# Optimization experiments

Hardware: AMD Instinct MI355X
Metric: run time of the kernel (lower is better)

Reference implementation:

```python
import jax, jax.numpy as jnp
import numpy as np


def _conv1x1(x, w, b):
    # x: [B,C,H,W], w: [O,C], b: [O] -> [B,O,H,W]
    return jnp.einsum('bchw,oc->bohw', x, w) + b[None, :, None, None]


def setup_inputs() -> dict:
    key = jax.random.key(0)
    ks = jax.random.split(key, 11)
    B, C, Ci, H, W = 4, 256, 128, 64, 64
    s_in = 1.0 / np.sqrt(C)
    s_ci = 1.0 / np.sqrt(Ci)
    return {
        'x': jax.random.normal(ks[0], (B, C, H, W), jnp.float32),
        'g_w': jax.random.normal(ks[1], (Ci, C), jnp.float32) * s_in,
        'g_b': jax.random.normal(ks[2], (Ci,), jnp.float32) * 0.01,
        'theta_w': jax.random.normal(ks[3], (Ci, C), jnp.float32) * s_in,
        'theta_b': jax.random.normal(ks[4], (Ci,), jnp.float32) * 0.01,
        'phi_w': jax.random.normal(ks[5], (Ci, C), jnp.float32) * s_in,
        'phi_b': jax.random.normal(ks[6], (Ci,), jnp.float32) * 0.01,
        'wz_w': jax.random.normal(ks[7], (C, Ci), jnp.float32) * s_ci,
        'wz_b': jax.random.normal(ks[8], (C,), jnp.float32) * 0.01,
        'bn_gamma': jax.random.uniform(ks[9], (C,), jnp.float32, 0.5, 1.5),
        'bn_beta': jax.random.normal(ks[10], (C,), jnp.float32) * 0.01,
    }


def reference(x, g_w, g_b, theta_w, theta_b, phi_w, phi_b, wz_w, wz_b, bn_gamma, bn_beta):
    B, C, H, W = x.shape
    Ci = g_w.shape[0]
    N = H * W
    # 1x1 conv projections, flattened over spatial positions
    g_x = _conv1x1(x, g_w, g_b).reshape(B, Ci, N).transpose(0, 2, 1)       # [B,N,Ci]
    theta_x = _conv1x1(x, theta_w, theta_b).reshape(B, Ci, N)              # [B,Ci,N]
    phi_x = _conv1x1(x, phi_w, phi_b).reshape(B, Ci, N)                    # [B,Ci,N]
    # f[b, i, j] = theta_i . phi_j  -> [B,N,N]
    f = jnp.einsum('bci,bcj->bij', theta_x, phi_x)
    # NOTE: softmax over dim=1 (query axis) — faithful to original (non-standard)
    f_div_C = jax.nn.softmax(f, axis=1)
    y = jnp.einsum('bij,bjc->bic', f_div_C, g_x)                           # [B,N,Ci]
    y = y.transpose(0, 2, 1).reshape(B, Ci, H, W)                          # [B,Ci,H,W]
    # W_z: 1x1 conv + BatchNorm2d (training-mode batch statistics)
    w_y = _conv1x1(y, wz_w, wz_b)                                          # [B,C,H,W]
    mean = jnp.mean(w_y, axis=(0, 2, 3), keepdims=True)
    var = jnp.var(w_y, axis=(0, 2, 3), keepdims=True)
    w_y = (w_y - mean) * jax.lax.rsqrt(var + 1e-5)
    w_y = w_y * bn_gamma[None, :, None, None] + bn_beta[None, :, None, None]
    return w_y + x
```

## Files before the change

kernel.cpp:

```cpp
#include <hip/hip_runtime.h>


#define B_  4
#define C_  256
#define CI  128
#define N_  4096
#define NB  (B_*N_)
#define ISPLIT 16
#define MB_ (1u<<20)
#define LOG2E 1.442695041f

typedef _Float16 f16;
typedef f16   f16x8 __attribute__((ext_vector_type(8)));
typedef f16   f16x4 __attribute__((ext_vector_type(4)));
typedef float f32x4 __attribute__((ext_vector_type(4)));
typedef float f32x16 __attribute__((ext_vector_type(16)));
typedef unsigned u32x2 __attribute__((ext_vector_type(2)));
typedef unsigned u32x4v __attribute__((ext_vector_type(4)));

#define MFMA(a,b,c)   __builtin_amdgcn_mfma_f32_16x16x32_f16(a,b,c,0,0,0)
#define MFMA32(a,b,c) __builtin_amdgcn_mfma_f32_32x32x16_f16(a,b,c,0,0,0)

#define GLD16(g, lp) __builtin_amdgcn_global_load_lds( \
    (const __attribute__((address_space(1))) void*)(g), \
    (__attribute__((address_space(3))) void*)(lp), 16, 0, 0)

#define OFF_THETA  0
#define OFF_PHI    (4u*MB_)
#define OFF_G      (8u*MB_)
#define OFF_YP     (12u*MB_)
#define OFF_WY     0
#define OFF_MD     (28u*MB_)
#define OFF_PS     (OFF_MD + 65536)
#define OFF_PSUM   (OFF_PS + ISPLIT*NB*4)
#define OFF_SSUM   (OFF_PSUM + 524288)
#define OFF_SSQ    (OFF_SSUM + 1024)
#define OFF_WCVT   (OFF_SSQ + 1024)
#define PSZ ((size_t)B_*N_*CI)

__global__ void k_init(const float* gw, const float* tw, const float* pw,
                       const float* zw, f16* wcvt) {
    int i = blockIdx.x * 256 + threadIdx.x;
    const float* s;
    int which = i >> 15;
    if (which == 0) s = gw; else if (which == 1) s = tw;
    else if (which == 2) s = pw; else s = zw;
    wcvt[i] = (f16)s[i & 32767];
}

__global__ __launch_bounds__(256) void k_proj(
        const float* __restrict__ x, const f16* __restrict__ wcvt,
        const float* __restrict__ gb, const float* __restrict__ tb,
        const float* __restrict__ pb,
        f16* __restrict__ thetaT, f16* __restrict__ phiT, f16* __restrict__ gC) {
    __shared__ __align__(16) f16 xT[32 * 264];
    int bb = blockIdx.x >> 7;
    int n0 = (blockIdx.x & 127) * 32;
    int t = threadIdx.x;

    const float* xb = x + (size_t)bb * C_ * N_;
    for (int rep = 0; rep < 8; rep++) {
        int lin = rep * 256 + t;
        int c = lin >> 3, np = (lin & 7) * 4;
        float4 v = *reinterpret_cast<const float4*>(xb + c * N_ + n0 + np);
        xT[(np + 0) * 264 + c] = (f16)v.x;
        xT[(np + 1) * 264 + c] = (f16)v.y;
        xT[(np + 2) * 264 + c] = (f16)v.z;
        xT[(np + 3) * 264 + c] = (f16)v.w;
    }
    __syncthreads();

    int w = t >> 6, l16 = t & 15, q = (t & 63) >> 4;
    int ci0 = w * 32;
    for (int proj = 0; proj < 3; proj++) {
        const f16* W0 = wcvt + proj * 32768;
        f32x4 acc[2][2] = {};
        for (int kk = 0; kk < 8; kk++) {
            f16x8 a0 = *reinterpret_cast<const f16x8*>(W0 + (ci0 + l16) * 256 + kk * 32 + q * 8);
            f16x8 a1 = *reinterpret_cast<const f16x8*>(W0 + (ci0 + 16 + l16) * 256 + kk * 32 + q * 8);
#pragma unroll
            for (int nt = 0; nt < 2; nt++) {
                f16x8 bv = *reinterpret_cast<const f16x8*>(&xT[(nt * 16 + l16) * 264 + kk * 32 + q * 8]);
                acc[0][nt] = MFMA(a0, bv, acc[0][nt]);
                acc[1][nt] = MFMA(a1, bv, acc[1][nt]);
            }
        }
        const float* bias = (proj == 0) ? gb : (proj == 1) ? tb : pb;
        float scl = (proj == 1) ? LOG2E : 1.0f;
#pragma unroll
        for (int a = 0; a < 2; a++) {
#pragma unroll
            for (int nt = 0; nt < 2; nt++) {
                int n = n0 + nt * 16 + l16;
                int cib = ci0 + a * 16 + q * 4;
                if (proj == 0) {
#pragma unroll
                    for (int r = 0; r < 4; r++)
                        gC[((size_t)bb * CI + cib + r) * N_ + n] = (f16)(acc[a][nt][r] + bias[cib + r]);
                } else {
                    f16x4 v4;
#pragma unroll
                    for (int r = 0; r < 4; r++)
                        v4[r] = (f16)((acc[a][nt][r] + bias[cib + r]) * scl);
                    f16* dst = (proj == 1 ? thetaT : phiT) + ((size_t)bb * N_ + n) * CI + cib;
                    *reinterpret_cast<f16x4*>(dst) = v4;
                }
            }
        }
    }
}

__global__ __launch_bounds__(256, 4) void k_cols(
        const f16* __restrict__ thetaT, const f16* __restrict__ phiT,
        float* __restrict__ ps) {
    __shared__ __align__(16) f16 thS[2][64 * 128];
    int id = blockIdx.x;
    int isp = id & 15, jb = (id >> 4) & 31, bb = id >> 9;
    int t = threadIdx.x, w = t >> 6, l = t & 63;
    int l31 = l & 31, hi = l >> 5;
    int jw = jb * 128 + w * 32 + l31;

    f16x8 pf[8];
    const f16* pb = phiT + ((size_t)bb * N_ + jw) * CI + hi * 8;
#pragma unroll
    for (int kk = 0; kk < 8; kk++)
        pf[kk] = *reinterpret_cast<const f16x8*>(pb + kk * 16);

    const f16* thB = thetaT + ((size_t)bb * N_ + isp * 256) * CI;
    auto stage = [&](int bf, int it0) {
#pragma unroll
        for (int r = 0; r < 4; r++) {
            int p = r * 256 + w * 64 + l;
            int pi = p >> 4, pu = (p & 15) ^ (pi & 15);
            const char* ga = (const char*)(thB + (size_t)(it0 + pi) * CI) + pu * 16;
            GLD16(ga, &thS[bf][(r * 256 + w * 64) * 8]);
        }
    };

    float s = 0.f;
    stage(0, 0);
    __syncthreads();
    for (int it = 0; it < 4; it++) {
        int bf = it & 1;
        if (it + 1 < 4) stage(bf ^ 1, (it + 1) * 64);
#pragma unroll
        for (int it2 = 0; it2 < 2; it2++) {
            f16x8 av[8];
#pragma unroll
            for (int kk = 0; kk < 8; kk++)
                av[kk] = *reinterpret_cast<const f16x8*>(
                    &thS[bf][(it2 * 32 + l31) * 128 + (((kk * 2 + hi) ^ (l31 & 15)) * 8)]);
            f32x16 f = {};
            __builtin_amdgcn_s_setprio(1);
#pragma unroll
            for (int kk = 0; kk < 8; kk++)
                f = MFMA32(av[kk], pf[kk], f);
            __builtin_amdgcn_s_setprio(0);
#pragma unroll
            for (int r = 0; r < 16; r++)
                s += __builtin_amdgcn_exp2f(f[r]);
        }
        __syncthreads();
    }
    s += __shfl_xor(s, 32);
    if (hi == 0)
        ps[isp * NB + bb * N_ + jw] = s;
}

__global__ void k_colmerge(const float* __restrict__ ps, float* __restrict__ md) {
    int j = blockIdx.x * 256 + threadIdx.x;
    float s = 0.f;
    for (int isp = 0; isp < ISPLIT; isp++) s += ps[isp * NB + j];
    md[j] = -__log2f(s);
}

__global__ __launch_bounds__(256, 2) void k_attn(
        const f16* __restrict__ thetaT, const f16* __restrict__ phiT,
        const f16* __restrict__ gC, const float* __restrict__ md,
        f16* __restrict__ yP) {
    __shared__ __align__(16) char smem[65536];
    f16 (*phiS)[64 * 128] = (f16(*)[64 * 128])smem;
    f16 (*gS)[128 * 64]   = (f16(*)[128 * 64])(smem + 32768);
    f16* yTr = (f16*)smem;

    int jq = blockIdx.x & 3;
    int ib = blockIdx.x >> 2;
    int bb = ib >> 5;
    int i0 = (ib & 31) * 128;
    int t = threadIdx.x, w = t >> 6, l = t & 63;
    int l31 = l & 31, hi = l >> 5;
    int jbase = jq * 1024;

    f16x8 ta[8];
    const f16* tb = thetaT + ((size_t)bb * N_ + i0 + w * 32 + l31) * CI + hi * 8;
#pragma unroll
    for (int kk = 0; kk < 8; kk++)
        ta[kk] = *reinterpret_cast<const f16x8*>(tb + kk * 16);

    const f16* phiB = phiT + (size_t)bb * N_ * CI;
    const f16* gB   = gC   + (size_t)bb * CI * N_;
    const float* mdb = md + bb * N_;

    auto stage = [&](int bf, int j0g) {
#pragma unroll
        for (int r = 0; r < 4; r++) {
            int p = r * 256 + w * 64 + l;
            int ub = (r * 256 + w * 64) * 8;
            int pj = p >> 4, pu = (p & 15) ^ (pj & 15);
            const char* ga = (const char*)(phiB + (size_t)(j0g + pj) * CI) + pu * 16;
            GLD16(ga, &phiS[bf][ub]);
            int pc = p >> 3, pu2 = (p & 7) ^ (pc & 7);
            const char* ga2 = (const char*)(gB + (size_t)pc * N_ + j0g) + pu2 * 16;
            GLD16(ga2, &gS[bf][ub]);
        }
    };

    f32x16 yacc[4] = {};
    stage(0, jbase);
    __syncthreads();
    for (int jt = 0; jt < 16; jt++) {
        int bf = jt & 1;
        if (jt + 1 < 16) stage(bf ^ 1, jbase + (jt + 1) * 64);

        f32x16 facc[2];
#pragma unroll
        for (int js = 0; js < 2; js++)
#pragma unroll
            for (int c = 0; c < 4; c++) {
                float4 v = *reinterpret_cast<const float4*>(
                    mdb + jbase + jt * 64 + js * 32 + c * 8 + hi * 4);
                facc[js][c * 4 + 0] = v.x; facc[js][c * 4 + 1] = v.y;
                facc[js][c * 4 + 2] = v.z; facc[js][c * 4 + 3] = v.w;
            }

        __builtin_amdgcn_s_setprio(1);
#pragma unroll
        for (int kk = 0; kk < 8; kk++) {
#pragma unroll
            for (int js = 0; js < 2; js++) {
                f16x8 pv = *reinterpret_cast<const f16x8*>(
                    &phiS[bf][(js * 32 + l31) * 128 + (((kk * 2 + hi) ^ (l31 & 15)) * 8)]);
                facc[js] = MFMA32(pv, ta[kk], facc[js]);
            }
        }
        __builtin_amdgcn_s_setprio(0);

#pragma unroll
        for (int js = 0; js < 2; js++) {
#pragma unroll
            for (int ch = 0; ch < 2; ch++) {
                float e0 = __builtin_amdgcn_exp2f(facc[js][ch * 8 + 0]);
                float e1 = __builtin_amdgcn_exp2f(facc[js][ch * 8 + 1]);
                float e2 = __builtin_amdgcn_exp2f(facc[js][ch * 8 + 2]);
                float e3 = __builtin_amdgcn_exp2f(facc[js][ch * 8 + 3]);
                float e4 = __builtin_amdgcn_exp2f(facc[js][ch * 8 + 4]);
                float e5 = __builtin_amdgcn_exp2f(facc[js][ch * 8 + 5]);
                float e6 = __builtin_amdgcn_exp2f(facc[js][ch * 8 + 6]);
                float e7 = __builtin_amdgcn_exp2f(facc[js][ch * 8 + 7]);
                unsigned p01 = __builtin_bit_cast(unsigned, __builtin_amdgcn_cvt_pkrtz(e0, e1));
                unsigned p23 = __builtin_bit_cast(unsigned, __builtin_amdgcn_cvt_pkrtz(e2, e3));
                unsigned p45 = __builtin_bit_cast(unsigned, __builtin_amdgcn_cvt_pkrtz(e4, e5));
                unsigned p67 = __builtin_bit_cast(unsigned, __builtin_amdgcn_cvt_pkrtz(e6, e7));
                u32x2 s0 = __builtin_amdgcn_permlane32_swap(p01, p45, false, false);
                u32x2 s1 = __builtin_amdgcn_permlane32_swap(p23, p67, false, false);
                u32x4v wu = {s0[0], s1[0], s0[1], s1[1]};
                f16x8 wfr = __builtin_bit_cast(f16x8, wu);
                int jc = js * 2 + ch;
                __builtin_amdgcn_s_setprio(1);
#pragma unroll
                for (int cs = 0; cs < 4; cs++) {
                    f16x8 gv = *reinterpret_cast<const f16x8*>(
                        &gS[bf][(cs * 32 + l31) * 64 + (((jc * 2 + hi) ^ (l31 & 7)) * 8)]);
                    yacc[cs] = MFMA32(wfr, gv, yacc[cs]);
                }
                __builtin_amdgcn_s_setprio(0);
            }
        }
        __syncthreads();
    }

    f16* yw = yTr + w * (32 * 136);
#pragma unroll
    for (int cs = 0; cs < 4; cs++)
#pragma unroll
        for (int r = 0; r < 16; r++)
            yw[((r & 3) + 8 * (r >> 2) + 4 * hi) * 136 + cs * 32 + l31] = (f16)yacc[cs][r];
    f16* yo = yP + (size_t)jq * PSZ + ((size_t)bb * N_ + i0 + w * 32) * CI;
#pragma unroll
    for (int rr = 0; rr < 8; rr++) {
        int chunk = rr * 64 + l;
        int il = chunk >> 4, u = chunk & 15;
        *reinterpret_cast<f16x8*>(yo + il * CI + u * 8) =
            *reinterpret_cast<const f16x8*>(&yw[il * 136 + u * 8]);
    }
}

__global__ __launch_bounds__(256) void k_wz(
        const f16* __restrict__ wzc, const f16* __restrict__ yP,
        const float* __restrict__ zb, f16* __restrict__ wy,
        float* __restrict__ psum) {
    int id = blockIdx.x;
    int nb = id & 63, bb = id >> 6;
    int t = threadIdx.x, w = t >> 6, l16 = t & 15, q = (t & 63) >> 4;
    int o0 = w * 64, n0 = nb * 64;
    f32x4 acc[4][4] = {};
#pragma unroll
    for (int kk = 0; kk < 4; kk++) {
        f16x8 bv[4];
#pragma unroll
        for (int nt = 0; nt < 4; nt++) {
            size_t yi = ((size_t)bb * N_ + n0 + nt * 16 + l16) * CI + kk * 32 + q * 8;
            f16x8 b0 = *reinterpret_cast<const f16x8*>(yP + yi);
            f16x8 b1 = *reinterpret_cast<const f16x8*>(yP + PSZ + yi);
            f16x8 b2 = *reinterpret_cast<const f16x8*>(yP + 2 * PSZ + yi);
            f16x8 b3 = *reinterpret_cast<const f16x8*>(yP + 3 * PSZ + yi);
            bv[nt] = (b0 + b1) + (b2 + b3);
        }
#pragma unroll
        for (int os = 0; os < 4; os++) {
            f16x8 av = *reinterpret_cast<const f16x8*>(
                wzc + (o0 + os * 16 + l16) * CI + kk * 32 + q * 8);
#pragma unroll
            for (int nt = 0; nt < 4; nt++)
                acc[os][nt] = MFMA(av, bv[nt], acc[os][nt]);
        }
    }
#pragma unroll
    for (int os = 0; os < 4; os++)
#pragma unroll
    for (int r = 0; r < 4; r++) {
        int o = o0 + os * 16 + q * 4 + r;
        float bias = zb[o];
        float sr = 0.f, qr = 0.f;
#pragma unroll
        for (int nt = 0; nt < 4; nt++) {
            float v = acc[os][nt][r] + bias;
            wy[((size_t)bb * C_ + o) * N_ + n0 + nt * 16 + l16] = (f16)v;
            sr += v; qr += v * v;
        }
#pragma unroll
        for (int off = 1; off < 16; off <<= 1) {
            sr += __shfl_xor(sr, off);
            qr += __shfl_xor(qr, off);
        }
        if (l16 == 0) {
            psum[(o * 2 + 0) * 256 + id] = sr;
            psum[(o * 2 + 1) * 256 + id] = qr;
        }
    }
}

__global__ void k_red(const float* __restrict__ psum, float* __restrict__ ssum,
                      float* __restrict__ ssq) {
    int b = blockIdx.x;
    int o = threadIdx.x;
    const float* src = psum + (o * 2 + b) * 256;
    float s = 0.f;
    for (int k = 0; k < 64; k++) {
        float4 v = reinterpret_cast<const float4*>(src)[k];
        s += v.x + v.y + v.z + v.w;
    }
    (b == 0 ? ssum : ssq)[o] = s;
}

__global__ void k_final(const f16* __restrict__ wy, const float* __restrict__ x,
                        const float* __restrict__ ssum, const float* __restrict__ ssq,
                        const float* __restrict__ gamma, const float* __restrict__ beta,
                        float* __restrict__ out) {
    int p = blockIdx.x * 256 + threadIdx.x;
    int c = (p >> 9) & 255;
    const float inv = 1.0f / 16384.0f;
    float mean = ssum[c] * inv;
    float var = ssq[c] * inv - mean * mean;
    float s = gamma[c] * rsqrtf(var + 1e-5f);
    float h = beta[c] - mean * s;
    f16x8 wv = reinterpret_cast<const f16x8*>(wy)[p];
    float4 x0 = reinterpret_cast<const float4*>(x)[2 * p];
    float4 x1 = reinterpret_cast<const float4*>(x)[2 * p + 1];
    float4 o0, o1;
    o0.x = (float)wv[0] * s + h + x0.x;
    o0.y = (float)wv[1] * s + h + x0.y;
    o0.z = (float)wv[2] * s + h + x0.z;
    o0.w = (float)wv[3] * s + h + x0.w;
    o1.x = (float)wv[4] * s + h + x1.x;
    o1.y = (float)wv[5] * s + h + x1.y;
    o1.z = (float)wv[6] * s + h + x1.z;
    o1.w = (float)wv[7] * s + h + x1.w;
    reinterpret_cast<float4*>(out)[2 * p] = o0;
    reinterpret_cast<float4*>(out)[2 * p + 1] = o1;
}

extern "C" void kernel_launch(void* const* d_in, const int* in_sizes, int n_in,
                              void* d_out, int out_size, void* d_ws, size_t ws_size,
                              hipStream_t stream) {
    const float* x     = (const float*)d_in[0];
    const float* gw    = (const float*)d_in[1];
    const float* gb    = (const float*)d_in[2];
    const float* tw    = (const float*)d_in[3];
    const float* tbv   = (const float*)d_in[4];
    const float* pw    = (const float*)d_in[5];
    const float* pb    = (const float*)d_in[6];
    const float* zw    = (const float*)d_in[7];
    const float* zb    = (const float*)d_in[8];
    const float* gamma = (const float*)d_in[9];
    const float* beta  = (const float*)d_in[10];

    char* ws = (char*)d_ws;
    f16* thetaT = (f16*)(ws + OFF_THETA);
    f16* phiT   = (f16*)(ws + OFF_PHI);
    f16* gC     = (f16*)(ws + OFF_G);
    f16* yP     = (f16*)(ws + OFF_YP);
    f16* wy     = (f16*)(ws + OFF_WY);
    f16* wcvt   = (f16*)(ws + OFF_WCVT);
    float* md   = (float*)(ws + OFF_MD);
    float* ps   = (float*)(ws + OFF_PS);
    float* psum = (float*)(ws + OFF_PSUM);
    float* ssum = (float*)(ws + OFF_SSUM);
    float* ssq  = (float*)(ws + OFF_SSQ);

    k_init<<<512, 256, 0, stream>>>(gw, tw, pw, zw, wcvt);
    k_proj<<<512, 256, 0, stream>>>(x, wcvt, gb, tbv, pb, thetaT, phiT, gC);
    k_cols<<<2048, 256, 0, stream>>>(thetaT, phiT, ps);
    k_colmerge<<<64, 256, 0, stream>>>(ps, md);
    k_attn<<<512, 256, 0, stream>>>(thetaT, phiT, gC, md, yP);
    k_wz<<<256, 256, 0, stream>>>(wcvt + 3 * 32768, yP, zb, wy, psum);
    k_red<<<2, 256, 0, stream>>>(psum, ssum, ssq);
    k_final<<<2048, 256, 0, stream>>>(wy, x, ssum, ssq, gamma, beta, (float*)d_out);
}
```

Measured before the change: 201.0 us.

## Double query rows per attention block to reuse staged phi and g tiles

```diff
diff --git a/kernel.cpp b/kernel.cpp
--- a/kernel.cpp
+++ b/kernel.cpp
@@ -174,7 +174,7 @@
     md[j] = -__log2f(s);
 }
 
-__global__ __launch_bounds__(256, 2) void k_attn(
+__global__ __launch_bounds__(256, 1) void k_attn(
         const f16* __restrict__ thetaT, const f16* __restrict__ phiT,
         const f16* __restrict__ gC, const float* __restrict__ md,
         f16* __restrict__ yP) {
@@ -185,17 +185,20 @@
 
     int jq = blockIdx.x & 3;
     int ib = blockIdx.x >> 2;
-    int bb = ib >> 5;
-    int i0 = (ib & 31) * 128;
+    int bb = ib >> 4;
+    int i0 = (ib & 15) * 256;
     int t = threadIdx.x, w = t >> 6, l = t & 63;
     int l31 = l & 31, hi = l >> 5;
     int jbase = jq * 1024;
 
-    f16x8 ta[8];
-    const f16* tb = thetaT + ((size_t)bb * N_ + i0 + w * 32 + l31) * CI + hi * 8;
-#pragma unroll
-    for (int kk = 0; kk < 8; kk++)
-        ta[kk] = *reinterpret_cast<const f16x8*>(tb + kk * 16);
+    f16x8 ta[2][8];
+#pragma unroll
+    for (int is = 0; is < 2; is++) {
+        const f16* tb = thetaT + ((size_t)bb * N_ + i0 + w * 64 + is * 32 + l31) * CI + hi * 8;
+#pragma unroll
+        for (int kk = 0; kk < 8; kk++)
+            ta[is][kk] = *reinterpret_cast<const f16x8*>(tb + kk * 16);
+    }
 
     const f16* phiB = phiT + (size_t)bb * N_ * CI;
     const f16* gB   = gC   + (size_t)bb * CI * N_;
@@ -215,83 +218,91 @@
         }
     };
 
-    f32x16 yacc[4] = {};
+    f32x16 yacc[2][4] = {};
     stage(0, jbase);
     __syncthreads();
     for (int jt = 0; jt < 16; jt++) {
         int bf = jt & 1;
         if (jt + 1 < 16) stage(bf ^ 1, jbase + (jt + 1) * 64);
 
-        f32x16 facc[2];
+        f32x16 facc[2][2];
 #pragma unroll
         for (int js = 0; js < 2; js++)
 #pragma unroll
             for (int c = 0; c < 4; c++) {
                 float4 v = *reinterpret_cast<const float4*>(
                     mdb + jbase + jt * 64 + js * 32 + c * 8 + hi * 4);
-                facc[js][c * 4 + 0] = v.x; facc[js][c * 4 + 1] = v.y;
-                facc[js][c * 4 + 2] = v.z; facc[js][c * 4 + 3] = v.w;
+                facc[0][js][c * 4 + 0] = v.x; facc[0][js][c * 4 + 1] = v.y;
+                facc[0][js][c * 4 + 2] = v.z; facc[0][js][c * 4 + 3] = v.w;
+                facc[1][js][c * 4 + 0] = v.x; facc[1][js][c * 4 + 1] = v.y;
+                facc[1][js][c * 4 + 2] = v.z; facc[1][js][c * 4 + 3] = v.w;
             }
 
-        __builtin_amdgcn_s_setprio(1);
 #pragma unroll
         for (int kk = 0; kk < 8; kk++) {
 #pragma unroll
             for (int js = 0; js < 2; js++) {
                 f16x8 pv = *reinterpret_cast<const f16x8*>(
                     &phiS[bf][(js * 32 + l31) * 128 + (((kk * 2 + hi) ^ (l31 & 15)) * 8)]);
-                facc[js] = MFMA32(pv, ta[kk], facc[js]);
+                facc[0][js] = MFMA32(pv, ta[0][kk], facc[0][js]);
+                facc[1][js] = MFMA32(pv, ta[1][kk], facc[1][js]);
             }
         }
-        __builtin_amdgcn_s_setprio(0);
 
 #pragma unroll
         for (int js = 0; js < 2; js++) {
 #pragma unroll
             for (int ch = 0; ch < 2; ch++) {
-                float e0 = __builtin_amdgcn_exp2f(facc[js][ch * 8 + 0]);
-                float e1 = __builtin_amdgcn_exp2f(facc[js][ch * 8 + 1]);
-                float e2 = __builtin_amdgcn_exp2f(facc[js][ch * 8 + 2]);
-                float e3 = __builtin_amdgcn_exp2f(facc[js][ch * 8 + 3]);
-                float e4 = __builtin_amdgcn_exp2f(facc[js][ch * 8 + 4]);
-                float e5 = __builtin_amdgcn_exp2f(facc[js][ch * 8 + 5]);
-                float e6 = __builtin_amdgcn_exp2f(facc[js][ch * 8 + 6]);
-                float e7 = __builtin_amdgcn_exp2f(facc[js][ch * 8 + 7]);
-                unsigned p01 = __builtin_bit_cast(unsigned, __builtin_amdgcn_cvt_pkrtz(e0, e1));
-                unsigned p23 = __builtin_bit_cast(unsigned, __builtin_amdgcn_cvt_pkrtz(e2, e3));
-                unsigned p45 = __builtin_bit_cast(unsigned, __builtin_amdgcn_cvt_pkrtz(e4, e5));
-                unsigned p67 = __builtin_bit_cast(unsigned, __builtin_amdgcn_cvt_pkrtz(e6, e7));
-                u32x2 s0 = __builtin_amdgcn_permlane32_swap(p01, p45, false, false);
-                u32x2 s1 = __builtin_amdgcn_permlane32_swap(p23, p67, false, false);
-                u32x4v wu = {s0[0], s1[0], s0[1], s1[1]};
-                f16x8 wfr = __builtin_bit_cast(f16x8, wu);
+                f16x8 wfr[2];
+#pragma unroll
+                for (int is = 0; is < 2; is++) {
+                    float e0 = __builtin_amdgcn_exp2f(facc[is][js][ch * 8 + 0]);
+                    float e1 = __builtin_amdgcn_exp2f(facc[is][js][ch * 8 + 1]);
+                    float e2 = __builtin_amdgcn_exp2f(facc[is][js][ch * 8 + 2]);
+                    float e3 = __builtin_amdgcn_exp2f(facc[is][js][ch * 8 + 3]);
+                    float e4 = __builtin_amdgcn_exp2f(facc[is][js][ch * 8 + 4]);
+                    float e5 = __builtin_amdgcn_exp2f(facc[is][js][ch * 8 + 5]);
+                    float e6 = __builtin_amdgcn_exp2f(facc[is][js][ch * 8 + 6]);
+                    float e7 = __builtin_amdgcn_exp2f(facc[is][js][ch * 8 + 7]);
+                    unsigned p01 = __builtin_bit_cast(unsigned, __builtin_amdgcn_cvt_pkrtz(e0, e1));
+                    unsigned p23 = __builtin_bit_cast(unsigned, __builtin_amdgcn_cvt_pkrtz(e2, e3));
+                    unsigned p45 = __builtin_bit_cast(unsigned, __builtin_amdgcn_cvt_pkrtz(e4, e5));
+                    unsigned p67 = __builtin_bit_cast(unsigned, __builtin_amdgcn_cvt_pkrtz(e6, e7));
+                    u32x2 s0 = __builtin_amdgcn_permlane32_swap(p01, p45, false, false);
+                    u32x2 s1 = __builtin_amdgcn_permlane32_swap(p23, p67, false, false);
+                    u32x4v wu = {s0[0], s1[0], s0[1], s1[1]};
+                    wfr[is] = __builtin_bit_cast(f16x8, wu);
+                }
                 int jc = js * 2 + ch;
-                __builtin_amdgcn_s_setprio(1);
 #pragma unroll
                 for (int cs = 0; cs < 4; cs++) {
                     f16x8 gv = *reinterpret_cast<const f16x8*>(
                         &gS[bf][(cs * 32 + l31) * 64 + (((jc * 2 + hi) ^ (l31 & 7)) * 8)]);
-                    yacc[cs] = MFMA32(wfr, gv, yacc[cs]);
+                    yacc[0][cs] = MFMA32(wfr[0], gv, yacc[0][cs]);
+                    yacc[1][cs] = MFMA32(wfr[1], gv, yacc[1][cs]);
                 }
-                __builtin_amdgcn_s_setprio(0);
             }
         }
         __syncthreads();
     }
 
-    f16* yw = yTr + w * (32 * 136);
-#pragma unroll
-    for (int cs = 0; cs < 4; cs++)
-#pragma unroll
-        for (int r = 0; r < 16; r++)
-            yw[((r & 3) + 8 * (r >> 2) + 4 * hi) * 136 + cs * 32 + l31] = (f16)yacc[cs][r];
-    f16* yo = yP + (size_t)jq * PSZ + ((size_t)bb * N_ + i0 + w * 32) * CI;
-#pragma unroll
-    for (int rr = 0; rr < 8; rr++) {
-        int chunk = rr * 64 + l;
-        int il = chunk >> 4, u = chunk & 15;
-        *reinterpret_cast<f16x8*>(yo + il * CI + u * 8) =
-            *reinterpret_cast<const f16x8*>(&yw[il * 136 + u * 8]);
+#pragma unroll
+    for (int is = 0; is < 2; is++) {
+        f16* yw = yTr + w * (32 * 136);
+#pragma unroll
+        for (int cs = 0; cs < 4; cs++)
+#pragma unroll
+            for (int r = 0; r < 16; r++)
+                yw[((r & 3) + 8 * (r >> 2) + 4 * hi) * 136 + cs * 32 + l31] = (f16)yacc[is][cs][r];
+        f16* yo = yP + (size_t)jq * PSZ + ((size_t)bb * N_ + i0 + w * 64 + is * 32) * CI;
+        __builtin_amdgcn_s_waitcnt(0);
+#pragma unroll
+        for (int rr = 0; rr < 8; rr++) {
+            int chunk = rr * 64 + l;
+            int il = chunk >> 4, u = chunk & 15;
+            *reinterpret_cast<f16x8*>(yo + il * CI + u * 8) =
+                *reinterpret_cast<const f16x8*>(&yw[il * 136 + u * 8]);
+        }
     }
 }
 
@@ -422,7 +433,7 @@
     k_proj<<<512, 256, 0, stream>>>(x, wcvt, gb, tbv, pb, thetaT, phiT, gC);
     k_cols<<<2048, 256, 0, stream>>>(thetaT, phiT, ps);
     k_colmerge<<<64, 256, 0, stream>>>(ps, md);
-    k_attn<<<512, 256, 0, stream>>>(thetaT, phiT, gC, md, yP);
+    k_attn<<<256, 256, 0, stream>>>(thetaT, phiT, gC, md, yP);
     k_wz<<<256, 256, 0, stream>>>(wcvt + 3 * 32768, yP, zb, wy, psum);
     k_red<<<2, 256, 0, stream>>>(psum, ssum, ssq);
     k_final<<<2048, 256, 0, stream>>>(wy, x, ssum, ssq, gamma, beta, (float*)d_out);
```

Result: no change. 204.3 us (+1.6%).
